# Kernel optimization log

Hardware: AMD Instinct MI355X
Metric: run time of the kernel (lower is better)

Reference implementation:

```python
import jax, jax.numpy as jnp
import numpy as np

S = 2048        # tokens (single prefill sequence)
HID = 3584      # hidden_size
H = 16          # num query heads
KV = 8          # num kv heads
D = 256         # head_dim
WINDOW = 1024   # sliding window size
CAP = 50.0      # logit softcap
SCALE = 256.0 ** -0.5   # query_pre_attn_scalar ** -0.5
THETA = 10000.0


def setup_inputs() -> dict:
    key = jax.random.key(0)
    ks = jax.random.split(key, 5)
    hidden_states = jax.random.normal(ks[0], (S, HID), dtype=jnp.float32)
    positions = jnp.arange(S, dtype=jnp.int32)
    Wq = jax.random.normal(ks[1], (HID, H * D), dtype=jnp.float32) * 0.02
    Wk = jax.random.normal(ks[2], (HID, KV * D), dtype=jnp.float32) * 0.02
    Wv = jax.random.normal(ks[3], (HID, KV * D), dtype=jnp.float32) * 0.02
    Wo = jax.random.normal(ks[4], (H * D, HID), dtype=jnp.float32) * 0.02
    return {"hidden_states": hidden_states, "positions": positions,
            "Wq": Wq, "Wk": Wk, "Wv": Wv, "Wo": Wo}


def _rope_neox(x, positions):
    # x: [S, n_heads, D]; neox-style: rotate halves, full rotary_dim == D
    half = D // 2
    inv_freq = 1.0 / (THETA ** (jnp.arange(0, half, dtype=jnp.float32) * 2.0 / D))
    freqs = positions.astype(jnp.float32)[:, None] * inv_freq[None, :]  # [S, half]
    cos = jnp.cos(freqs)[:, None, :].astype(x.dtype)
    sin = jnp.sin(freqs)[:, None, :].astype(x.dtype)
    x1, x2 = x[..., :half], x[..., half:]
    return jnp.concatenate([x1 * cos - x2 * sin, x2 * cos + x1 * sin], axis=-1)


def reference(hidden_states, positions, Wq, Wk, Wv, Wo):
    # QKV projections (no bias)
    q = (hidden_states @ Wq).reshape(S, H, D)
    k = (hidden_states @ Wk).reshape(S, KV, D)
    v = (hidden_states @ Wv).reshape(S, KV, D)
    q = _rope_neox(q, positions)
    k = _rope_neox(k, positions)
    # grouped-query attention: G query heads per kv head
    G = H // KV
    qg = q.reshape(S, KV, G, D)
    scores = jnp.einsum('qkgd,skd->kgqs', qg, k) * jnp.asarray(SCALE, q.dtype)
    # logit soft-capping
    scores = CAP * jnp.tanh(scores / CAP)
    # causal + sliding-window mask
    i = positions[:, None]
    j = positions[None, :]
    mask = (j <= i) & ((i - j) < WINDOW)   # [S, S]
    neg = jnp.finfo(scores.dtype).min
    scores = jnp.where(mask[None, None, :, :], scores, neg)
    p = jax.nn.softmax(scores, axis=-1)
    attn = jnp.einsum('kgqs,skd->qkgd', p, v).reshape(S, H * D)
    return attn @ Wo
```

## Files before the change

kernel.cpp:

```cpp
#include <hip/hip_runtime.h>
#include <stdint.h>

#define S 2048
#define HID 3584
#define NH 16
#define NKV 8
#define DH 256
#define WINDOW 1024
#define SCALE 0.0625f
#define CAP 50.0f

typedef short s16x8 __attribute__((ext_vector_type(8)));
typedef float f32x4 __attribute__((ext_vector_type(4)));

__device__ __forceinline__ short f2bf(float f) {
  union { float f; uint32_t u; } c; c.f = f;
  uint32_t u = c.u;
  uint32_t r = (u + 0x7FFFu + ((u >> 16) & 1u)) >> 16;
  return (short)r;
}
__device__ __forceinline__ float bf2f(short s) {
  union { uint32_t u; float f; } c;
  c.u = ((uint32_t)(uint16_t)s) << 16;
  return c.f;
}
__device__ __forceinline__ void gll16(const void* g, void* l) {
  __builtin_amdgcn_global_load_lds((const __attribute__((address_space(1))) void*)g,
                                   (__attribute__((address_space(3))) void*)l, 16, 0, 0);
}

__global__ void rope_table_kernel(float2* __restrict__ tbl) {
  int idx = blockIdx.x * 256 + threadIdx.x;
  int s = idx >> 7, i = idx & 127;
  float inv = __expf(-(float)i * (9.210340371976184f / 128.0f));
  float fr = (float)s * inv;
  tbl[idx] = make_float2(cosf(fr), sinf(fr));
}

__global__ void conv_hs_kernel(const float* __restrict__ src, short* __restrict__ dst) {
  int gid = blockIdx.x * 256 + threadIdx.x;
  float4 a = *(const float4*)&src[(size_t)gid * 8];
  float4 b = *(const float4*)&src[(size_t)gid * 8 + 4];
  s16x8 o;
  o[0] = f2bf(a.x); o[1] = f2bf(a.y); o[2] = f2bf(a.z); o[3] = f2bf(a.w);
  o[4] = f2bf(b.x); o[5] = f2bf(b.y); o[6] = f2bf(b.z); o[7] = f2bf(b.w);
  *(s16x8*)&dst[(size_t)gid * 8] = o;
}

__global__ __launch_bounds__(256)
void transpose_all_kernel(const float* __restrict__ Wq, const float* __restrict__ Wk,
                          const float* __restrict__ Wv, const float* __restrict__ Wo,
                          short* __restrict__ Wt, short* __restrict__ WtO)
{
  __shared__ __align__(16) short t[64][76];
  int b = blockIdx.x;
  const float* src; short* dst; int K, N, lb;
  if (b < 3584)      { src = Wq; dst = Wt;                       K = HID;  N = 4096; lb = b; }
  else if (b < 5376) { src = Wk; dst = Wt + (size_t)4096 * HID;  K = HID;  N = 2048; lb = b - 3584; }
  else if (b < 7168) { src = Wv; dst = Wt + (size_t)6144 * HID;  K = HID;  N = 2048; lb = b - 5376; }
  else               { src = Wo; dst = WtO;                      K = 4096; N = HID;  lb = b - 7168; }
  int ntn = N >> 6;
  int tn = lb % ntn, tk = lb / ntn;
  int tid = threadIdx.x;
  int c = tid & 63, rg = tid >> 6;
  #pragma unroll
  for (int i = 0; i < 4; ++i) {
    int r0 = i * 16 + rg * 4;
    short tmp[4];
    #pragma unroll
    for (int j = 0; j < 4; ++j)
      tmp[j] = f2bf(src[(size_t)(tk * 64 + r0 + j) * N + tn * 64 + c]);
    *(short4*)&t[c][r0] = *(short4*)tmp;
  }
  __syncthreads();
  #pragma unroll
  for (int it = 0; it < 2; ++it) {
    int flat = it * 256 + tid;
    int n = flat >> 3, kc = flat & 7;
    *(s16x8*)&dst[(size_t)(tn * 64 + n) * K + tk * 64 + kc * 8] = *(s16x8*)&t[n][kc * 8];
  }
}

__global__ __launch_bounds__(256, 2)
void qkv_gemm_kernel(const short* __restrict__ hsb, const short* __restrict__ Wt,
                     short* __restrict__ qb, short* __restrict__ kbuf,
                     short* __restrict__ vtb)
{
  __shared__ __align__(16) short Asb[256 * 64];
  __shared__ __align__(16) short Bsb[128 * 64];
  int bid = blockIdx.x;
  int i = bid >> 3;
  int bm = i & 7;
  int bn = (bid & 7) * 8 + (i >> 3);
  int m0 = bm * 256, n0 = bn * 128;
  int tid = threadIdx.x, w = tid >> 6, lane = tid & 63;
  int lr = lane & 15, lk = lane >> 4;
  int wm = (w >> 1) * 128, wn = (w & 1) * 64;
  int r7 = lr & 7;
  int abase = (wm + lr) * 64 + ((lk ^ r7) * 8);
  int bbase = (wn + lr) * 64 + ((lk ^ r7) * 8);
  int row8 = tid >> 3;
  int colsw = ((tid & 7) ^ (row8 & 7)) * 8;
  const short* srcA = hsb + (size_t)(m0 + row8) * HID + colsw;
  const short* srcB = Wt + (size_t)(n0 + row8) * HID + colsw;
  f32x4 acc[8][4] = {};
  for (int t = 0; t < HID / 64; ++t) {
    const short* sa = srcA + t * 64;
    const short* sb = srcB + t * 64;
    #pragma unroll
    for (int r = 0; r < 8; ++r)
      gll16(sa + (size_t)(r * 32) * HID, Asb + r * 2048 + w * 512);
    #pragma unroll
    for (int r = 0; r < 4; ++r)
      gll16(sb + (size_t)(r * 32) * HID, Bsb + r * 2048 + w * 512);
    __syncthreads();
    s16x8 bf[4][2];
    #pragma unroll
    for (int nf = 0; nf < 4; ++nf)
      #pragma unroll
      for (int kh = 0; kh < 2; ++kh)
        bf[nf][kh] = *(const s16x8*)&Bsb[(bbase + nf * 16 * 64) ^ (kh * 32)];
    #pragma unroll
    for (int mh = 0; mh < 2; ++mh) {
      s16x8 af[4][2];
      #pragma unroll
      for (int mf = 0; mf < 4; ++mf)
        #pragma unroll
        for (int kh = 0; kh < 2; ++kh)
          af[mf][kh] = *(const s16x8*)&Asb[(abase + (mh * 64 + mf * 16) * 64) ^ (kh * 32)];
      __builtin_amdgcn_s_setprio(1);
      #pragma unroll
      for (int mf = 0; mf < 4; ++mf)
        #pragma unroll
        for (int nf = 0; nf < 4; ++nf) {
          acc[mh * 4 + mf][nf] = __builtin_amdgcn_mfma_f32_16x16x32_bf16(
              af[mf][0], bf[nf][0], acc[mh * 4 + mf][nf], 0, 0, 0);
          acc[mh * 4 + mf][nf] = __builtin_amdgcn_mfma_f32_16x16x32_bf16(
              af[mf][1], bf[nf][1], acc[mh * 4 + mf][nf], 0, 0, 0);
        }
      __builtin_amdgcn_s_setprio(0);
    }
    __syncthreads();
  }
  int region = (n0 < 4096) ? 0 : ((n0 < 6144) ? 1 : 2);
  #pragma unroll
  for (int m = 0; m < 8; ++m) {
    int srow_b = m0 + wm + m * 16 + lk * 4;
    #pragma unroll
    for (int n = 0; n < 4; ++n) {
      int ncol = n0 + wn + n * 16 + lr;
      #pragma unroll
      for (int r = 0; r < 4; ++r) {
        int srow = srow_b + r;
        short bv = f2bf(acc[m][n][r]);
        if (region == 0) {
          int h = ncol >> 8, d = ncol & 255;
          qb[((size_t)h * S + srow) * DH + d] = bv;
        } else if (region == 1) {
          int c = ncol - 4096; int kv = c >> 8, d = c & 255;
          kbuf[((size_t)kv * S + srow) * DH + d] = bv;
        } else {
          int c = ncol - 6144; int kv = c >> 8, d = c & 255;
          vtb[((size_t)kv * DH + d) * S + srow] = bv;
        }
      }
    }
  }
}

__global__ __launch_bounds__(256)
void out_gemm_kernel(const short* __restrict__ attnb, const short* __restrict__ WtO,
                     float* __restrict__ out)
{
  __shared__ __align__(16) short Asb[128 * 64];
  __shared__ __align__(16) short Bsb[128 * 64];
  int bid = blockIdx.x;
  int flat = (bid & 7) * 56 + (bid >> 3);
  int bn = flat >> 4, bm = flat & 15;
  int m0 = bm * 128, n0 = bn * 128;
  int tid = threadIdx.x, w = tid >> 6, lane = tid & 63;
  int lr = lane & 15, lk = lane >> 4;
  int wm = (w >> 1) * 64, wn = (w & 1) * 64;
  int r7 = lr & 7;
  int abase = (wm + lr) * 64 + ((lk ^ r7) * 8);
  int bbase = (wn + lr) * 64 + ((lk ^ r7) * 8);
  int row8 = tid >> 3;
  int colsw = ((tid & 7) ^ (row8 & 7)) * 8;
  const short* srcA = attnb + (size_t)(m0 + row8) * 4096 + colsw;
  const short* srcB = WtO + (size_t)(n0 + row8) * 4096 + colsw;
  f32x4 acc[4][4] = {};
  for (int t = 0; t < 4096 / 64; ++t) {
    const short* sa = srcA + t * 64;
    const short* sb = srcB + t * 64;
    #pragma unroll
    for (int r = 0; r < 4; ++r)
      gll16(sa + (size_t)(r * 32) * 4096, Asb + r * 2048 + w * 512);
    #pragma unroll
    for (int r = 0; r < 4; ++r)
      gll16(sb + (size_t)(r * 32) * 4096, Bsb + r * 2048 + w * 512);
    __syncthreads();
    s16x8 af[4][2], bf[4][2];
    #pragma unroll
    for (int f = 0; f < 4; ++f)
      #pragma unroll
      for (int kh = 0; kh < 2; ++kh) {
        af[f][kh] = *(const s16x8*)&Asb[(abase + f * 16 * 64) ^ (kh * 32)];
        bf[f][kh] = *(const s16x8*)&Bsb[(bbase + f * 16 * 64) ^ (kh * 32)];
      }
    __builtin_amdgcn_s_setprio(1);
    #pragma unroll
    for (int mf = 0; mf < 4; ++mf)
      #pragma unroll
      for (int nf = 0; nf < 4; ++nf) {
        acc[mf][nf] = __builtin_amdgcn_mfma_f32_16x16x32_bf16(
            af[mf][0], bf[nf][0], acc[mf][nf], 0, 0, 0);
        acc[mf][nf] = __builtin_amdgcn_mfma_f32_16x16x32_bf16(
            af[mf][1], bf[nf][1], acc[mf][nf], 0, 0, 0);
      }
    __builtin_amdgcn_s_setprio(0);
    __syncthreads();
  }
  #pragma unroll
  for (int mf = 0; mf < 4; ++mf) {
    int srow_b = m0 + wm + mf * 16 + lk * 4;
    #pragma unroll
    for (int nf = 0; nf < 4; ++nf) {
      int ncol = n0 + wn + nf * 16 + lr;
      #pragma unroll
      for (int r = 0; r < 4; ++r)
        out[(size_t)(srow_b + r) * HID + ncol] = acc[mf][nf][r];
    }
  }
}

__global__ void rope_kernel(short* __restrict__ qb, short* __restrict__ kbuf,
                            const float2* __restrict__ tbl)
{
  int gid = blockIdx.x * 256 + threadIdx.x;
  int row = gid >> 4, ch = gid & 15;
  short* base = (row < NH * S) ? (qb + (size_t)row * DH)
                               : (kbuf + (size_t)(row - NH * S) * DH);
  int s = row & (S - 1);
  int i0 = ch * 8;
  s16x8 x1 = *(s16x8*)(base + i0);
  s16x8 x2 = *(s16x8*)(base + 128 + i0);
  s16x8 y1, y2;
  #pragma unroll
  for (int j = 0; j < 8; ++j) {
    float2 cs = tbl[s * 128 + i0 + j];
    float a = bf2f(x1[j]), b = bf2f(x2[j]);
    y1[j] = f2bf(a * cs.x - b * cs.y);
    y2[j] = f2bf(b * cs.x + a * cs.y);
  }
  *(s16x8*)(base + i0) = y1;
  *(s16x8*)(base + 128 + i0) = y2;
}

__global__ __launch_bounds__(512)
void attn_kernel(const short* __restrict__ qb, const short* __restrict__ kbuf,
                 const short* __restrict__ vtb, short* __restrict__ attnb)
{
  __shared__ __align__(16) short Klds[2][64][256];
  __shared__ __align__(16) short Vlds[2][256][64];
  __shared__ __align__(16) short Plds[8][16][72];
  int bid = blockIdx.x;
  int qt = 31 - (bid >> 4), h = bid & 15;
  int kv = h >> 1;
  int q0 = qt * 64;
  int tid = threadIdx.x;
  int w = tid >> 6, lane = tid & 63;
  int g = w >> 2, wsub = w & 3;
  int gtid = tid & 255;
  int lr = lane & 15, lk = lane >> 4;
  int qrow_base = q0 + wsub * 16;
  s16x8 qf[8];
  const short* qrow = qb + ((size_t)h * S + (qrow_base + lr)) * DH;
  #pragma unroll
  for (int kb = 0; kb < 8; ++kb)
    qf[kb] = *(const s16x8*)(qrow + kb * 32 + lk * 8);
  f32x4 acc_o[16] = {};
  float l_r[4] = {0.0f, 0.0f, 0.0f, 0.0f};
  int tlo = (q0 >= WINDOW - 1) ? ((q0 - (WINDOW - 1)) >> 6) : 0;
  int thi = q0 >> 6;
  const short* kbase = kbuf + (size_t)kv * S * DH;
  const short* vbase = vtb + (size_t)kv * DH * S;

  s16x8 kpf[8], vpf[8];
  auto loadRegs = [&](int t) {
    int k0 = t * 64;
    #pragma unroll
    for (int it = 0; it < 8; ++it) {
      int flat = it * 256 + gtid;
      int r = flat >> 5, cg = flat & 31;
      kpf[it] = *(const s16x8*)(kbase + (size_t)(k0 + r) * DH + cg * 8);
    }
    #pragma unroll
    for (int it = 0; it < 8; ++it) {
      int flat = it * 256 + gtid;
      int r = flat >> 3, cg = flat & 7;
      vpf[it] = *(const s16x8*)(vbase + (size_t)r * S + k0 + cg * 8);
    }
  };
  auto writeLds = [&]() {
    #pragma unroll
    for (int it = 0; it < 8; ++it) {
      int flat = it * 256 + gtid;
      int r = flat >> 5, cg = flat & 31;
      *(s16x8*)&Klds[g][r][(cg ^ (r & 7)) * 8] = kpf[it];
    }
    #pragma unroll
    for (int it = 0; it < 8; ++it) {
      int flat = it * 256 + gtid;
      int r = flat >> 3, cg = flat & 7;
      *(s16x8*)&Vlds[g][r][(cg ^ (r & 7)) * 8] = vpf[it];
    }
  };

  int tg0 = tlo + g;
  int n_all = thi - tlo + 1;
  int jmax = (n_all + 1) >> 1;
  if (tg0 <= thi) loadRegs(tg0);
  for (int j = 0; j < jmax; ++j) {
    int t = tg0 + 2 * j;
    bool active = (t <= thi);
    if (active) writeLds();
    __syncthreads();
    if (active && t + 2 <= thi) loadRegs(t + 2);
    if (active) {
      int k0 = t * 64;
      f32x4 sc4[4] = {};
      __builtin_amdgcn_s_setprio(1);
      #pragma unroll
      for (int kb = 0; kb < 8; ++kb)
        #pragma unroll
        for (int ni = 0; ni < 4; ++ni) {
          int row = ni * 16 + lr;
          s16x8 b = *(const s16x8*)&Klds[g][row][(((kb << 2) | lk) ^ (row & 7)) * 8];
          sc4[ni] = __builtin_amdgcn_mfma_f32_16x16x32_bf16(qf[kb], b, sc4[ni], 0, 0, 0);
        }
      __builtin_amdgcn_s_setprio(0);
      bool interior = (k0 + 63 <= qrow_base) && (qrow_base + 15 - k0 < WINDOW);
      #pragma unroll
      for (int ni = 0; ni < 4; ++ni)
        #pragma unroll
        for (int r = 0; r < 4; ++r) {
          float raw = sc4[ni][r];
          float e = __expf(-fabsf(raw) * (2.0f * SCALE / CAP));
          float wgt = raw > 0.0f ? e : 1.0f;
          float p = __expf(-2.0f * CAP * __fdividef(wgt, 1.0f + e));
          if (!interior) {
            int qg = qrow_base + lk * 4 + r;
            int kg = k0 + ni * 16 + lr;
            bool valid = (kg <= qg) && (qg - kg < WINDOW);
            p = valid ? p : 0.0f;
          }
          sc4[ni][r] = p;
          l_r[r] += p;
        }
      #pragma unroll
      for (int ni = 0; ni < 4; ++ni)
        #pragma unroll
        for (int r = 0; r < 4; ++r)
          Plds[w][lk * 4 + r][ni * 16 + lr] = f2bf(sc4[ni][r]);
      s16x8 pa0 = *(const s16x8*)&Plds[w][lr][lk * 8];
      s16x8 pa1 = *(const s16x8*)&Plds[w][lr][32 + lk * 8];
      __builtin_amdgcn_s_setprio(1);
      #pragma unroll
      for (int df = 0; df < 16; ++df) {
        int row = df * 16 + lr;
        s16x8 b0 = *(const s16x8*)&Vlds[g][row][((lk ^ (row & 7)) * 8)];
        s16x8 b1 = *(const s16x8*)&Vlds[g][row][(((4 + lk) ^ (row & 7)) * 8)];
        acc_o[df] = __builtin_amdgcn_mfma_f32_16x16x32_bf16(pa0, b0, acc_o[df], 0, 0, 0);
        acc_o[df] = __builtin_amdgcn_mfma_f32_16x16x32_bf16(pa1, b1, acc_o[df], 0, 0, 0);
      }
      __builtin_amdgcn_s_setprio(0);
    }
    __syncthreads();
  }
  float lsum[4];
  #pragma unroll
  for (int r = 0; r < 4; ++r) {
    float v = l_r[r];
    #pragma unroll
    for (int off = 1; off < 16; off <<= 1)
      v += __shfl_xor(v, off, 64);
    lsum[r] = v;
  }
  float* comb = (float*)&Klds[0][0][0];
  float* lcomb = (float*)&Vlds[0][0][0];
  if (g == 1) {
    #pragma unroll
    for (int df = 0; df < 16; ++df)
      #pragma unroll
      for (int r = 0; r < 4; ++r)
        comb[(size_t)(wsub * 16 + lk * 4 + r) * 256 + df * 16 + lr] = acc_o[df][r];
    if (lr == 0)
      #pragma unroll
      for (int r = 0; r < 4; ++r)
        lcomb[wsub * 16 + lk * 4 + r] = lsum[r];
  }
  __syncthreads();
  if (g == 0) {
    #pragma unroll
    for (int r = 0; r < 4; ++r) {
      int rowi = wsub * 16 + lk * 4 + r;
      float lt = lsum[r] + lcomb[rowi];
      float inv = 1.0f / lt;
      int srow = q0 + rowi;
      #pragma unroll
      for (int df = 0; df < 16; ++df) {
        float o = acc_o[df][r] + comb[(size_t)rowi * 256 + df * 16 + lr];
        attnb[(size_t)srow * (NH * DH) + h * DH + df * 16 + lr] = f2bf(o * inv);
      }
    }
  }
}

extern "C" void kernel_launch(void* const* d_in, const int* in_sizes, int n_in,
                              void* d_out, int out_size, void* d_ws, size_t ws_size,
                              hipStream_t stream) {
  const float* hs = (const float*)d_in[0];
  const float* Wq = (const float*)d_in[2];
  const float* Wk = (const float*)d_in[3];
  const float* Wv = (const float*)d_in[4];
  const float* Wo = (const float*)d_in[5];
  float* out = (float*)d_out;
  char* ws = (char*)d_ws;
  size_t off = 0;
  float2* tbl  = (float2*)(ws + off); off += 2097152;
  short* qb    = (short*)(ws + off);  off += 16777216;
  short* kbuf  = (short*)(ws + off);  off += 8388608;
  short* vtb   = (short*)(ws + off);  off += 8388608;
  short* attnb = (short*)(ws + off);  off += 16777216;
  short* hsb   = (short*)(ws + off);  off += 14680064;
  short* Wt    = (short*)(ws + off);  off += 58720256;
  short* WtO   = (short*)(ws + off);  off += 29360128;

  hipLaunchKernelGGL(rope_table_kernel, dim3(1024), dim3(256), 0, stream, tbl);
  hipLaunchKernelGGL(conv_hs_kernel, dim3(3584), dim3(256), 0, stream, hs, hsb);
  hipLaunchKernelGGL(transpose_all_kernel, dim3(10752), dim3(256), 0, stream,
                     Wq, Wk, Wv, Wo, Wt, WtO);
  hipLaunchKernelGGL(qkv_gemm_kernel, dim3(512), dim3(256), 0, stream,
                     hsb, Wt, qb, kbuf, vtb);
  hipLaunchKernelGGL(rope_kernel, dim3(3072), dim3(256), 0, stream, qb, kbuf, tbl);
  hipLaunchKernelGGL(attn_kernel, dim3(512), dim3(512), 0, stream,
                     qb, kbuf, vtb, attnb);
  hipLaunchKernelGGL(out_gemm_kernel, dim3(448), dim3(256), 0, stream,
                     attnb, WtO, out);
}
```

Before: 377.6 us.

## Double-buffer LDS in shared GEMM helper and shrink QKV tile to 128x128

Factors the QKV and output GEMM main loops into a shared templated helper that double-buffers the LDS tiles. The next K-tile's global-to-LDS loads are issued before computing on the current one, with a single waitcnt+barrier per iteration instead of two syncthreads. The QKV GEMM tile shrinks from 256x128 to 128x128, doubling the grid to 1024 blocks with fewer accumulators per thread. This trades more A/B reloads for better occupancy and load overlap. The out GEMM also gets a min-2-blocks launch bound.

Result: slower. 392.3 us (+3.9%).

```diff
diff --git a/kernel.cpp b/kernel.cpp
--- a/kernel.cpp
+++ b/kernel.cpp
@@ -81,78 +81,94 @@
   }
 }
 
+template<int KS>
+__device__ __forceinline__ void gemm_t3(const short* __restrict__ srcA,
+                                        const short* __restrict__ srcB,
+                                        int tid, int NT, f32x4 (&acc)[4][4])
+{
+  __shared__ __align__(16) short Asb[2][128 * 64];
+  __shared__ __align__(16) short Bsb[2][128 * 64];
+  const int w = tid >> 6, lane = tid & 63;
+  const int lr = lane & 15, lk = lane >> 4;
+  const int wm = (w >> 1) * 64, wn = (w & 1) * 64;
+  const int r7 = lr & 7;
+  const int abase = (wm + lr) * 64 + ((lk ^ r7) * 8);
+  const int bbase = (wn + lr) * 64 + ((lk ^ r7) * 8);
+
+  auto stage = [&](int t, int b) {
+    const short* sa = srcA + (size_t)t * 64;
+    const short* sb = srcB + (size_t)t * 64;
+    #pragma unroll
+    for (int r = 0; r < 4; ++r)
+      gll16(sa + (size_t)(r * 32) * KS, &Asb[b][r * 2048 + w * 512]);
+    #pragma unroll
+    for (int r = 0; r < 4; ++r)
+      gll16(sb + (size_t)(r * 32) * KS, &Bsb[b][r * 2048 + w * 512]);
+  };
+
+  stage(0, 0);
+  asm volatile("s_waitcnt vmcnt(0)" ::: "memory");
+  asm volatile("s_barrier" ::: "memory");
+
+  for (int t = 0; t < NT; ++t) {
+    const int cur = t & 1;
+    if (t + 1 < NT) stage(t + 1, cur ^ 1);
+    s16x8 af[4][2], bf[4][2];
+    #pragma unroll
+    for (int f = 0; f < 4; ++f)
+      #pragma unroll
+      for (int kh = 0; kh < 2; ++kh) {
+        af[f][kh] = *(const s16x8*)&Asb[cur][(abase + f * 16 * 64) ^ (kh * 32)];
+        bf[f][kh] = *(const s16x8*)&Bsb[cur][(bbase + f * 16 * 64) ^ (kh * 32)];
+      }
+    __builtin_amdgcn_s_setprio(1);
+    #pragma unroll
+    for (int mf = 0; mf < 4; ++mf)
+      #pragma unroll
+      for (int nf = 0; nf < 4; ++nf) {
+        acc[mf][nf] = __builtin_amdgcn_mfma_f32_16x16x32_bf16(
+            af[mf][0], bf[nf][0], acc[mf][nf], 0, 0, 0);
+        acc[mf][nf] = __builtin_amdgcn_mfma_f32_16x16x32_bf16(
+            af[mf][1], bf[nf][1], acc[mf][nf], 0, 0, 0);
+      }
+    __builtin_amdgcn_s_setprio(0);
+    asm volatile("s_waitcnt vmcnt(0)" ::: "memory");
+    asm volatile("s_barrier" ::: "memory");
+  }
+}
+
 __global__ __launch_bounds__(256, 2)
 void qkv_gemm_kernel(const short* __restrict__ hsb, const short* __restrict__ Wt,
                      short* __restrict__ qb, short* __restrict__ kbuf,
                      short* __restrict__ vtb)
 {
-  __shared__ __align__(16) short Asb[256 * 64];
-  __shared__ __align__(16) short Bsb[128 * 64];
   int bid = blockIdx.x;
   int i = bid >> 3;
-  int bm = i & 7;
-  int bn = (bid & 7) * 8 + (i >> 3);
-  int m0 = bm * 256, n0 = bn * 128;
-  int tid = threadIdx.x, w = tid >> 6, lane = tid & 63;
-  int lr = lane & 15, lk = lane >> 4;
-  int wm = (w >> 1) * 128, wn = (w & 1) * 64;
-  int r7 = lr & 7;
-  int abase = (wm + lr) * 64 + ((lk ^ r7) * 8);
-  int bbase = (wn + lr) * 64 + ((lk ^ r7) * 8);
+  int bn = (bid & 7) * 8 + (i & 7);
+  int bm = i >> 3;
+  int m0 = bm * 128, n0 = bn * 128;
+  int tid = threadIdx.x;
   int row8 = tid >> 3;
   int colsw = ((tid & 7) ^ (row8 & 7)) * 8;
   const short* srcA = hsb + (size_t)(m0 + row8) * HID + colsw;
   const short* srcB = Wt + (size_t)(n0 + row8) * HID + colsw;
-  f32x4 acc[8][4] = {};
-  for (int t = 0; t < HID / 64; ++t) {
-    const short* sa = srcA + t * 64;
-    const short* sb = srcB + t * 64;
-    #pragma unroll
-    for (int r = 0; r < 8; ++r)
-      gll16(sa + (size_t)(r * 32) * HID, Asb + r * 2048 + w * 512);
-    #pragma unroll
-    for (int r = 0; r < 4; ++r)
-      gll16(sb + (size_t)(r * 32) * HID, Bsb + r * 2048 + w * 512);
-    __syncthreads();
-    s16x8 bf[4][2];
-    #pragma unroll
-    for (int nf = 0; nf < 4; ++nf)
-      #pragma unroll
-      for (int kh = 0; kh < 2; ++kh)
-        bf[nf][kh] = *(const s16x8*)&Bsb[(bbase + nf * 16 * 64) ^ (kh * 32)];
-    #pragma unroll
-    for (int mh = 0; mh < 2; ++mh) {
-      s16x8 af[4][2];
-      #pragma unroll
-      for (int mf = 0; mf < 4; ++mf)
-        #pragma unroll
-        for (int kh = 0; kh < 2; ++kh)
-          af[mf][kh] = *(const s16x8*)&Asb[(abase + (mh * 64 + mf * 16) * 64) ^ (kh * 32)];
-      __builtin_amdgcn_s_setprio(1);
-      #pragma unroll
-      for (int mf = 0; mf < 4; ++mf)
-        #pragma unroll
-        for (int nf = 0; nf < 4; ++nf) {
-          acc[mh * 4 + mf][nf] = __builtin_amdgcn_mfma_f32_16x16x32_bf16(
-              af[mf][0], bf[nf][0], acc[mh * 4 + mf][nf], 0, 0, 0);
-          acc[mh * 4 + mf][nf] = __builtin_amdgcn_mfma_f32_16x16x32_bf16(
-              af[mf][1], bf[nf][1], acc[mh * 4 + mf][nf], 0, 0, 0);
-        }
-      __builtin_amdgcn_s_setprio(0);
-    }
-    __syncthreads();
-  }
+  f32x4 acc[4][4] = {};
+  gemm_t3<HID>(srcA, srcB, tid, HID / 64, acc);
+
+  int w = tid >> 6, lane = tid & 63;
+  int lr = lane & 15, lk = lane >> 4;
+  int wm = (w >> 1) * 64, wn = (w & 1) * 64;
   int region = (n0 < 4096) ? 0 : ((n0 < 6144) ? 1 : 2);
   #pragma unroll
-  for (int m = 0; m < 8; ++m) {
-    int srow_b = m0 + wm + m * 16 + lk * 4;
-    #pragma unroll
-    for (int n = 0; n < 4; ++n) {
-      int ncol = n0 + wn + n * 16 + lr;
+  for (int mf = 0; mf < 4; ++mf) {
+    int srow_b = m0 + wm + mf * 16 + lk * 4;
+    #pragma unroll
+    for (int nf = 0; nf < 4; ++nf) {
+      int ncol = n0 + wn + nf * 16 + lr;
       #pragma unroll
       for (int r = 0; r < 4; ++r) {
         int srow = srow_b + r;
-        short bv = f2bf(acc[m][n][r]);
+        short bv = f2bf(acc[mf][nf][r]);
         if (region == 0) {
           int h = ncol >> 8, d = ncol & 255;
           qb[((size_t)h * S + srow) * DH + d] = bv;
@@ -168,58 +184,25 @@
   }
 }
 
-__global__ __launch_bounds__(256)
+__global__ __launch_bounds__(256, 2)
 void out_gemm_kernel(const short* __restrict__ attnb, const short* __restrict__ WtO,
                      float* __restrict__ out)
 {
-  __shared__ __align__(16) short Asb[128 * 64];
-  __shared__ __align__(16) short Bsb[128 * 64];
   int bid = blockIdx.x;
   int flat = (bid & 7) * 56 + (bid >> 3);
   int bn = flat >> 4, bm = flat & 15;
   int m0 = bm * 128, n0 = bn * 128;
-  int tid = threadIdx.x, w = tid >> 6, lane = tid & 63;
-  int lr = lane & 15, lk = lane >> 4;
-  int wm = (w >> 1) * 64, wn = (w & 1) * 64;
-  int r7 = lr & 7;
-  int abase = (wm + lr) * 64 + ((lk ^ r7) * 8);
-  int bbase = (wn + lr) * 64 + ((lk ^ r7) * 8);
+  int tid = threadIdx.x;
   int row8 = tid >> 3;
   int colsw = ((tid & 7) ^ (row8 & 7)) * 8;
   const short* srcA = attnb + (size_t)(m0 + row8) * 4096 + colsw;
   const short* srcB = WtO + (size_t)(n0 + row8) * 4096 + colsw;
   f32x4 acc[4][4] = {};
-  for (int t = 0; t < 4096 / 64; ++t) {
-    const short* sa = srcA + t * 64;
-    const short* sb = srcB + t * 64;
-    #pragma unroll
-    for (int r = 0; r < 4; ++r)
-      gll16(sa + (size_t)(r * 32) * 4096, Asb + r * 2048 + w * 512);
-    #pragma unroll
-    for (int r = 0; r < 4; ++r)
-      gll16(sb + (size_t)(r * 32) * 4096, Bsb + r * 2048 + w * 512);
-    __syncthreads();
-    s16x8 af[4][2], bf[4][2];
-    #pragma unroll
-    for (int f = 0; f < 4; ++f)
-      #pragma unroll
-      for (int kh = 0; kh < 2; ++kh) {
-        af[f][kh] = *(const s16x8*)&Asb[(abase + f * 16 * 64) ^ (kh * 32)];
-        bf[f][kh] = *(const s16x8*)&Bsb[(bbase + f * 16 * 64) ^ (kh * 32)];
-      }
-    __builtin_amdgcn_s_setprio(1);
-    #pragma unroll
-    for (int mf = 0; mf < 4; ++mf)
-      #pragma unroll
-      for (int nf = 0; nf < 4; ++nf) {
-        acc[mf][nf] = __builtin_amdgcn_mfma_f32_16x16x32_bf16(
-            af[mf][0], bf[nf][0], acc[mf][nf], 0, 0, 0);
-        acc[mf][nf] = __builtin_amdgcn_mfma_f32_16x16x32_bf16(
-            af[mf][1], bf[nf][1], acc[mf][nf], 0, 0, 0);
-      }
-    __builtin_amdgcn_s_setprio(0);
-    __syncthreads();
-  }
+  gemm_t3<4096>(srcA, srcB, tid, 4096 / 64, acc);
+
+  int w = tid >> 6, lane = tid & 63;
+  int lr = lane & 15, lk = lane >> 4;
+  int wm = (w >> 1) * 64, wn = (w & 1) * 64;
   #pragma unroll
   for (int mf = 0; mf < 4; ++mf) {
     int srow_b = m0 + wm + mf * 16 + lk * 4;
@@ -440,7 +423,7 @@
   hipLaunchKernelGGL(conv_hs_kernel, dim3(3584), dim3(256), 0, stream, hs, hsb);
   hipLaunchKernelGGL(transpose_all_kernel, dim3(10752), dim3(256), 0, stream,
                      Wq, Wk, Wv, Wo, Wt, WtO);
-  hipLaunchKernelGGL(qkv_gemm_kernel, dim3(512), dim3(256), 0, stream,
+  hipLaunchKernelGGL(qkv_gemm_kernel, dim3(1024), dim3(256), 0, stream,
                      hsb, Wt, qb, kbuf, vtb);
   hipLaunchKernelGGL(rope_kernel, dim3(3072), dim3(256), 0, stream, qb, kbuf, tbl);
   hipLaunchKernelGGL(attn_kernel, dim3(512), dim3(512), 0, stream,
```
